# Kernel tuning notes

Measured on AMD Instinct MI355X. Metric: run time of the kernel, lower is better.

Reference implementation:

```python
import jax, jax.numpy as jnp
import numpy as np

B, T, D = 32, 1024, 512
H = 1024          # hidden_size
LV = 128          # level_hidden_size
NREP = H // LV    # n_repeat = 8
NL = 2            # num_layers


def setup_inputs() -> dict:
    key = jax.random.key(0)
    ks = jax.random.split(key, 9)
    s = 0.02
    inp = {"x": jax.random.normal(ks[0], (B, T, D), jnp.float32)}
    # layer 0: input dim D; layer 1: input dim H
    inp["W_lstm0"] = jax.random.normal(ks[1], (4 * H, D + H), jnp.float32) * s
    inp["b_lstm0"] = jnp.zeros((4 * H,), jnp.float32)
    inp["W_lvl0"] = jax.random.normal(ks[2], (2 * LV, D + H), jnp.float32) * s
    inp["b_lvl0"] = jnp.zeros((2 * LV,), jnp.float32)
    inp["W_lstm1"] = jax.random.normal(ks[3], (4 * H, H + H), jnp.float32) * s
    inp["b_lstm1"] = jnp.zeros((4 * H,), jnp.float32)
    inp["W_lvl1"] = jax.random.normal(ks[4], (2 * LV, H + H), jnp.float32) * s
    inp["b_lvl1"] = jnp.zeros((2 * LV,), jnp.float32)
    return inp


def _cell(Wl, bl, Wv, bv, h, c, x_t):
    comb = jnp.concatenate([x_t, h], axis=-1)               # [B, in+H]
    gates = comb @ Wl.T + bl                                 # [B, 4H]
    cc_i, cc_f, cc_o, cc_g = jnp.split(gates, 4, axis=-1)
    lvl = comb @ Wv.T + bv                                   # [B, 2*LV]
    cc_i_h, cc_f_h = jnp.split(lvl, 2, axis=-1)
    i = jax.nn.sigmoid(cc_i)
    f = jax.nn.sigmoid(cc_f)
    o = jax.nn.sigmoid(cc_o)
    g = jnp.tanh(cc_g)
    p_f = jax.nn.softmax(cc_f_h, axis=-1)
    p_i = jax.nn.softmax(cc_i_h[..., ::-1], axis=-1)
    i_h = jnp.cumsum(p_f, axis=-1)                           # master input gate
    f_h = jnp.cumsum(p_i, axis=-1)[..., ::-1]                # master forget gate
    i_h = jnp.repeat(i_h, NREP, axis=-1)                     # [B, H]
    f_h = jnp.repeat(f_h, NREP, axis=-1)
    w = i_h * f_h
    c_new = w * (f * c + i * g) + (f_h - w) * c + (i_h - w) * g
    h_new = o * jnp.tanh(c_new)
    return h_new, c_new


def _run_layer(Wl, bl, Wv, bv, x):
    # x: [B, T, in]
    bsz = x.shape[0]
    h0 = jnp.zeros((bsz, H), x.dtype)
    c0 = jnp.zeros((bsz, H), x.dtype)

    def step(carry, x_t):
        h, c = carry
        h, c = _cell(Wl, bl, Wv, bv, h, c, x_t)
        return (h, c), h

    (_, _), hs = jax.lax.scan(step, (h0, c0), jnp.swapaxes(x, 0, 1))
    return jnp.swapaxes(hs, 0, 1)                            # [B, T, H]


def reference(x, W_lstm0, b_lstm0, W_lvl0, b_lvl0,
              W_lstm1, b_lstm1, W_lvl1, b_lvl1):
    out0 = _run_layer(W_lstm0, b_lstm0, W_lvl0, b_lvl0, x)
    out1 = _run_layer(W_lstm1, b_lstm1, W_lvl1, b_lvl1, out0)
    return out1
```

## Files before the change

kernel.cpp:

```cpp
#include <hip/hip_runtime.h>

namespace {
constexpr int kB  = 32;
constexpr int kT  = 1024;
constexpr int kD  = 512;
constexpr int kH  = 1024;
constexpr int kLV = 128;
constexpr int kNG = 4 * kH + 2 * kLV;
constexpr int kNBLK = 256;
constexpr int kNTHR = 512;
constexpr int kOffH0 = 8192;
constexpr int kOffWF = kOffH0 + 2 * kB * kH + 2 * kB * kNG;
constexpr int kRedOff = 3 * 1536 * 2 * 16;
constexpr int kIhOff  = kRedOff + 6144;
constexpr int kFhOff  = kIhOff + 512;
constexpr int kSmxOff = kFhOff + 512;
constexpr int kLdsBytes = kSmxOff + 32;
}

typedef float vfloat4 __attribute__((ext_vector_type(4)));
typedef float floatx4 __attribute__((ext_vector_type(4)));
typedef _Float16 half8_t __attribute__((ext_vector_type(8)));
typedef unsigned short ushort_t;

static __device__ __forceinline__ unsigned ld_flag(const unsigned* p) {
  return __hip_atomic_load(p, __ATOMIC_RELAXED, __HIP_MEMORY_SCOPE_AGENT);
}
static __device__ __forceinline__ void st_flag(unsigned* p, unsigned v) {
  __hip_atomic_store(p, v, __ATOMIC_RELAXED, __HIP_MEMORY_SCOPE_AGENT);
}
static __device__ __forceinline__ float ld_coh(const float* p) {
  return __hip_atomic_load(p, __ATOMIC_RELAXED, __HIP_MEMORY_SCOPE_AGENT);
}
static __device__ __forceinline__ void st_wt(float* p, float v) {
  asm volatile("global_store_dword %0, %1, off sc0 sc1" :: "v"(p), "v"(v) : "memory");
}
static __device__ __forceinline__ void st_wtu(unsigned* p, unsigned v) {
  asm volatile("global_store_dword %0, %1, off sc0 sc1" :: "v"(p), "v"(v) : "memory");
}
static __device__ __forceinline__ void ld8h(uint4 v[8], const ushort_t* b) {
  asm volatile(
      "global_load_dwordx4 %0, %8, off sc0 sc1\n\t"
      "global_load_dwordx4 %1, %8, off offset:256 sc0 sc1\n\t"
      "global_load_dwordx4 %2, %8, off offset:512 sc0 sc1\n\t"
      "global_load_dwordx4 %3, %8, off offset:768 sc0 sc1\n\t"
      "global_load_dwordx4 %4, %8, off offset:1024 sc0 sc1\n\t"
      "global_load_dwordx4 %5, %8, off offset:1280 sc0 sc1\n\t"
      "global_load_dwordx4 %6, %8, off offset:1536 sc0 sc1\n\t"
      "global_load_dwordx4 %7, %8, off offset:1792 sc0 sc1\n\t"
      "s_waitcnt vmcnt(0)"
      : "=&v"(v[0]), "=&v"(v[1]), "=&v"(v[2]), "=&v"(v[3]),
        "=&v"(v[4]), "=&v"(v[5]), "=&v"(v[6]), "=&v"(v[7])
      : "v"(b)
      : "memory");
}
static __device__ __forceinline__ void ld8h2(uint4 v[8], uint4 w[8],
                                             const ushort_t* b0, const ushort_t* b1) {
  asm volatile(
      "global_load_dwordx4 %0,  %16, off sc0 sc1\n\t"
      "global_load_dwordx4 %1,  %16, off offset:256 sc0 sc1\n\t"
      "global_load_dwordx4 %2,  %16, off offset:512 sc0 sc1\n\t"
      "global_load_dwordx4 %3,  %16, off offset:768 sc0 sc1\n\t"
      "global_load_dwordx4 %4,  %16, off offset:1024 sc0 sc1\n\t"
      "global_load_dwordx4 %5,  %16, off offset:1280 sc0 sc1\n\t"
      "global_load_dwordx4 %6,  %16, off offset:1536 sc0 sc1\n\t"
      "global_load_dwordx4 %7,  %16, off offset:1792 sc0 sc1\n\t"
      "global_load_dwordx4 %8,  %17, off sc0 sc1\n\t"
      "global_load_dwordx4 %9,  %17, off offset:256 sc0 sc1\n\t"
      "global_load_dwordx4 %10, %17, off offset:512 sc0 sc1\n\t"
      "global_load_dwordx4 %11, %17, off offset:768 sc0 sc1\n\t"
      "global_load_dwordx4 %12, %17, off offset:1024 sc0 sc1\n\t"
      "global_load_dwordx4 %13, %17, off offset:1280 sc0 sc1\n\t"
      "global_load_dwordx4 %14, %17, off offset:1536 sc0 sc1\n\t"
      "global_load_dwordx4 %15, %17, off offset:1792 sc0 sc1\n\t"
      "s_waitcnt vmcnt(0)"
      : "=&v"(v[0]), "=&v"(v[1]), "=&v"(v[2]), "=&v"(v[3]),
        "=&v"(v[4]), "=&v"(v[5]), "=&v"(v[6]), "=&v"(v[7]),
        "=&v"(w[0]), "=&v"(w[1]), "=&v"(w[2]), "=&v"(w[3]),
        "=&v"(w[4]), "=&v"(w[5]), "=&v"(w[6]), "=&v"(w[7])
      : "v"(b0), "v"(b1)
      : "memory");
}
static __device__ __forceinline__ unsigned pkrtz(float a, float b) {
  return __builtin_bit_cast(unsigned, __builtin_amdgcn_cvt_pkrtz(a, b));
}
static __device__ __forceinline__ uint4 pack2(vfloat4 a, vfloat4 b) {
  uint4 r;
  r.x = pkrtz(a.x, a.y); r.y = pkrtz(a.z, a.w);
  r.z = pkrtz(b.x, b.y); r.w = pkrtz(b.z, b.w);
  return r;
}
static __device__ __forceinline__ floatx4 mfma16(uint4 a, uint4 b, floatx4 c) {
  return __builtin_amdgcn_mfma_f32_16x16x32_f16(
      __builtin_bit_cast(half8_t, a), __builtin_bit_cast(half8_t, b), c, 0, 0, 0);
}

__global__ __launch_bounds__(256) void cvt_fp16_kernel(
    const float* __restrict__ src, ushort_t* __restrict__ dst, int n8) {
  int i = blockIdx.x * 256 + threadIdx.x;
  if (i >= n8) return;
  const vfloat4* s4 = (const vfloat4*)src;
  vfloat4 a = s4[2 * i], b = s4[2 * i + 1];
  typedef _Float16 h8 __attribute__((ext_vector_type(8)));
  h8 o;
  o[0] = (_Float16)a.x; o[1] = (_Float16)a.y;
  o[2] = (_Float16)a.z; o[3] = (_Float16)a.w;
  o[4] = (_Float16)b.x; o[5] = (_Float16)b.y;
  o[6] = (_Float16)b.z; o[7] = (_Float16)b.w;
  ((h8*)dst)[i] = o;
}

__global__ __launch_bounds__(kNTHR, 2) void onlstm_kernel(
    const float* __restrict__ x,
    const float* __restrict__ bl0, const float* __restrict__ bv0,
    const float* __restrict__ bl1, const float* __restrict__ bv1,
    const ushort_t* __restrict__ wf0u, const ushort_t* __restrict__ wf1u,
    float* __restrict__ out, float* __restrict__ ws)
{
  const int tid = threadIdx.x;
  const int bid = blockIdx.x;

  unsigned* flags = (unsigned*)ws;
  unsigned* genp  = (unsigned*)ws + 4096;
  ushort_t* h0f = (ushort_t*)(ws + kOffH0);
  ushort_t* h1f = h0f + kB * kH;
  float* gates0 = ws + kOffH0 + kB * kH;
  float* gates1 = gates0 + kB * kNG;

  __shared__ __align__(16) char sb[kLdsBytes];
  uint4* wb4   = (uint4*)sb;
  float* redp  = (float*)(sb + kRedOff);
  float* ih_sh = (float*)(sb + kIhOff);
  float* fh_sh = (float*)(sb + kFhOff);
  float* smx   = (float*)(sb + kSmxOff);

  unsigned seq = 0;
  auto gridbar = [&]() {
    ++seq;
    asm volatile("s_waitcnt vmcnt(0)" ::: "memory");
    __syncthreads();
    if (bid == 0) {
      if (tid >= 1 && tid < kNBLK) {
        while (ld_flag(&flags[tid * 16]) != seq) __builtin_amdgcn_s_sleep(2);
      }
      __syncthreads();
      if (tid == 0) st_flag(genp, seq);
    } else {
      if (tid == 0) {
        st_flag(&flags[bid * 16], seq);
        while (ld_flag(genp) != seq) __builtin_amdgcn_s_sleep(2);
      }
      __syncthreads();
    }
    asm volatile("" ::: "memory");
  };

  int L, ntile, cb0;
  if (bid < 32)       { L = 0; ntile = 3; cb0 = bid * 48; }
  else if (bid < 120) { L = 0; ntile = 2; cb0 = 1536 + (bid - 32) * 32; }
  else                { L = 1; ntile = 2; cb0 = (bid - 120) * 32; }
  const int K   = L ? 2048 : 1536;
  const int ts4 = K * 2;
  const bool three = (ntile == 3);
  const ushort_t* wf = L ? wf1u : wf0u;
  const float* blp = L ? bl1 : bl0;
  const float* bvp = L ? bv1 : bv0;
  float* gatesL = L ? gates1 : gates0;

  const int lane = tid & 63;
  const int rt   = (tid >> 6) & 1;
  const int str  = tid >> 7;
  const int r_   = rt * 16 + (lane & 15);
  const int koct = lane >> 4;
  const int colg0 = cb0 + (lane & 15);
  const int colg1 = cb0 + 16 + (lane & 15);
  const int colg2 = cb0 + 32 + (lane & 15);

  for (int tt = 0; tt < ntile; ++tt) {
    const int colb = cb0 + tt * 16;
    for (int idx = tid; idx < ts4; idx += kNTHR) {
      int m = idx >> 6, l2 = idx & 63;
      size_t off = (size_t)(colb + (l2 & 15)) * K + m * 32 + 8 * (l2 >> 4);
      wb4[tt * ts4 + idx] = *(const uint4*)(wf + off);
    }
  }
  const float b0w = (colg0 < 4096) ? blp[colg0] : bvp[colg0 - 4096];
  const float b1w = (colg1 < 4096) ? blp[colg1] : bvp[colg1 - 4096];
  const float b2w = three ? ((colg2 < 4096) ? blp[colg2] : bvp[colg2 - 4096]) : 0.f;
  __syncthreads();

  { int idx = bid * kNTHR + tid; if (idx < kB * kH) st_wtu((unsigned*)h0f + idx, 0u); }
  float creg = 0.f;
  gridbar();

  const int pbB  = (bid & 127) >> 2;
  const int qq4B = bid & 3;
  auto cellB = [&](const float* gbase, ushort_t* hb, float& cr, float* outp, int t) {
    const float* gr = gbase + (size_t)pbB * kNG;
    const int wl = tid & 63, wv2 = tid >> 6;
    const bool sm = tid < 128;
    const bool cl = tid < 256;
    float vi = 0.f, vf = 0.f, vo = 0.f, vg = 0.f;
    int j = qq4B * 256 + tid;
    if (cl) {
      vi = ld_coh(gr + j);
      vf = ld_coh(gr + kH + j);
      vo = ld_coh(gr + 2 * kH + j);
      vg = ld_coh(gr + 3 * kH + j);
    }
    float ai = 0.f, af = 0.f;
    if (sm) { ai = ld_coh(gr + 4096 + tid); af = ld_coh(gr + 4096 + kLV + tid); }
    float mi = ai, mf = af;
    if (sm) {
#pragma unroll
      for (int d2 = 32; d2 > 0; d2 >>= 1) {
        mi = fmaxf(mi, __shfl_xor(mi, d2));
        mf = fmaxf(mf, __shfl_xor(mf, d2));
      }
      if (wl == 0) { smx[wv2] = mi; smx[2 + wv2] = mf; }
    }
    __syncthreads();
    mi = fmaxf(smx[0], smx[1]);
    mf = fmaxf(smx[2], smx[3]);
    float ei = 0.f, Pi = 0.f, Pf = 0.f;
    if (sm) {
      ei = __expf(ai - mi);
      float ef = __expf(af - mf);
      Pi = ei; Pf = ef;
#pragma unroll
      for (int d2 = 1; d2 < 64; d2 <<= 1) {
        float ni = __shfl_up(Pi, d2);
        float nf = __shfl_up(Pf, d2);
        if (wl >= d2) { Pi += ni; Pf += nf; }
      }
      if (wl == 63) { smx[4 + wv2] = Pi; smx[6 + wv2] = Pf; }
    }
    __syncthreads();
    float Si = smx[4] + smx[5], Sf = smx[6] + smx[7];
    if (sm) {
      if (wv2 == 1) { Pi += smx[4]; Pf += smx[6]; }
      ih_sh[tid] = Pf / Sf;
      fh_sh[tid] = (Si - Pi + ei) / Si;
    }
    __syncthreads();
    if (cl) {
      float i_ = 1.f / (1.f + __expf(-vi));
      float f_ = 1.f / (1.f + __expf(-vf));
      float o_ = 1.f / (1.f + __expf(-vo));
      float g_ = tanhf(vg);
      int l2 = j >> 3;
      float ih = ih_sh[l2], fh = fh_sh[l2];
      float w  = ih * fh;
      float cold = cr;
      float cn = w * (f_ * cold + i_ * g_) + (fh - w) * cold + (ih - w) * g_;
      float hn = o_ * tanhf(cn);
      cr = cn;
      float hnn = __shfl_xor(hn, 1);
      if (!(tid & 1))
        st_wtu((unsigned*)hb + ((size_t)pbB * kH + j) / 2, pkrtz(hn, hnn));
      if (outp) st_wt(outp + ((size_t)pbB * kT + t) * kH + j, hn);
    }
  };

  for (int e = 0; e <= kT; ++e) {
    const bool actA = L ? (e >= 1) : (e < kT);

    if (actA) {
      floatx4 a0 = {0.f,0.f,0.f,0.f}, a1 = a0, a2 = a0;
      if (L == 0) {
        {
          const float* bx = x + ((size_t)r_ * kT + e) * kD + str * 32 + koct * 8;
          vfloat4 vx[8];
#pragma unroll
          for (int j = 0; j < 4; ++j) {
            vx[2*j]   = *(const vfloat4*)(bx + j * 128);
            vx[2*j+1] = *(const vfloat4*)(bx + j * 128 + 4);
          }
          uint4 pa[4];
#pragma unroll
          for (int j = 0; j < 4; ++j) pa[j] = pack2(vx[2*j], vx[2*j+1]);
#pragma unroll
          for (int j = 0; j < 4; ++j) {
            const int m = str + 4 * j;
            a0 = mfma16(pa[j], wb4[m * 64 + lane], a0);
            a1 = mfma16(pa[j], wb4[ts4 + m * 64 + lane], a1);
            if (three) a2 = mfma16(pa[j], wb4[2 * ts4 + m * 64 + lane], a2);
          }
        }
        {
          uint4 pa[8];
          ld8h(pa, h0f + (size_t)r_ * kH + str * 32 + koct * 8);
#pragma unroll
          for (int j = 0; j < 8; ++j) {
            const int m = 16 + str + 4 * j;
            a0 = mfma16(pa[j], wb4[m * 64 + lane], a0);
            a1 = mfma16(pa[j], wb4[ts4 + m * 64 + lane], a1);
            if (three) a2 = mfma16(pa[j], wb4[2 * ts4 + m * 64 + lane], a2);
          }
        }
      } else {
        uint4 pa[8], pb[8];
        ld8h2(pa, pb, h0f + (size_t)r_ * kH + str * 32 + koct * 8,
                      h1f + (size_t)r_ * kH + str * 32 + koct * 8);
#pragma unroll
        for (int j = 0; j < 8; ++j) {
          const int m = str + 4 * j;
          a0 = mfma16(pa[j], wb4[m * 64 + lane], a0);
          a1 = mfma16(pa[j], wb4[ts4 + m * 64 + lane], a1);
        }
#pragma unroll
        for (int j = 0; j < 8; ++j) {
          const int m = 32 + str + 4 * j;
          a0 = mfma16(pb[j], wb4[m * 64 + lane], a0);
          a1 = mfma16(pb[j], wb4[ts4 + m * 64 + lane], a1);
        }
      }
      for (int s2 = 1; s2 < 4; ++s2) {
        if (str == s2) {
          *(floatx4*)&redp[((rt * 3 + 0) * 64 + lane) * 4] = a0;
          *(floatx4*)&redp[((rt * 3 + 1) * 64 + lane) * 4] = a1;
          if (three) *(floatx4*)&redp[((rt * 3 + 2) * 64 + lane) * 4] = a2;
        }
        __syncthreads();
        if (str == 0) {
          a0 += *(const floatx4*)&redp[((rt * 3 + 0) * 64 + lane) * 4];
          a1 += *(const floatx4*)&redp[((rt * 3 + 1) * 64 + lane) * 4];
          if (three) a2 += *(const floatx4*)&redp[((rt * 3 + 2) * 64 + lane) * 4];
        }
        __syncthreads();
      }
      if (str == 0) {
        const int rb = rt * 16 + koct * 4;
#pragma unroll
        for (int r = 0; r < 4; ++r)
          st_wt(gatesL + (size_t)(rb + r) * kNG + colg0, a0[r] + b0w);
#pragma unroll
        for (int r = 0; r < 4; ++r)
          st_wt(gatesL + (size_t)(rb + r) * kNG + colg1, a1[r] + b1w);
        if (three) {
#pragma unroll
          for (int r = 0; r < 4; ++r)
            st_wt(gatesL + (size_t)(rb + r) * kNG + colg2, a2[r] + b2w);
        }
      }
    }
    gridbar();

    if (bid < 128) {
      if (e < kT) cellB(gates0, h0f, creg, nullptr, e);
    } else {
      if (e >= 1) cellB(gates1, h1f, creg, out, e - 1);
    }
    gridbar();
  }
}

extern "C" void kernel_launch(void* const* d_in, const int* in_sizes, int n_in,
                              void* d_out, int out_size, void* d_ws, size_t ws_size,
                              hipStream_t stream) {
  const float* x   = (const float*)d_in[0];
  const float* Wl0 = (const float*)d_in[1];
  const float* bl0 = (const float*)d_in[2];
  const float* Wv0 = (const float*)d_in[3];
  const float* bv0 = (const float*)d_in[4];
  const float* Wl1 = (const float*)d_in[5];
  const float* bl1 = (const float*)d_in[6];
  const float* Wv1 = (const float*)d_in[7];
  const float* bv1 = (const float*)d_in[8];
  (void)in_sizes; (void)n_in; (void)out_size; (void)ws_size;

  float* ws = (float*)d_ws;
  ushort_t* wf0 = (ushort_t*)(ws + kOffWF);
  ushort_t* wf1 = wf0 + (size_t)4352 * 1536;

  {
    int n;
    n = 4096 * 1536 / 8;
    cvt_fp16_kernel<<<(n + 255) / 256, 256, 0, stream>>>(Wl0, wf0, n);
    n = 256 * 1536 / 8;
    cvt_fp16_kernel<<<(n + 255) / 256, 256, 0, stream>>>(
        Wv0, wf0 + (size_t)4096 * 1536, n);
    n = 4096 * 2048 / 8;
    cvt_fp16_kernel<<<(n + 255) / 256, 256, 0, stream>>>(Wl1, wf1, n);
    n = 256 * 2048 / 8;
    cvt_fp16_kernel<<<(n + 255) / 256, 256, 0, stream>>>(
        Wv1, wf1 + (size_t)4096 * 2048, n);
  }

  onlstm_kernel<<<dim3(kNBLK), dim3(kNTHR), 0, stream>>>(
      x, bl0, bv0, bl1, bv1, wf0, wf1, (float*)d_out, ws);
}
```

Baseline: 11.12 ms.

## Replace centralized grid barrier with per-block flag waits on dependent subsets

The single master-block grid barrier is replaced with per-block signal flags. Each block now polls only the flags of the blocks whose outputs it depends on: layer-0 GEMM blocks wait on the layer-0 cell blocks, and layer-1 blocks wait on all blocks or on layer-1 gate producers. This removes the two-hop gather-then-broadcast latency and some unnecessary waits each timestep. Separately, the cross-wave partial-sum reduction now uses multiple LDS slots so three waves write at once instead of serializing across three barrier rounds, at the cost of a doubled reduction buffer. Correctness relies on the dependency subsets and monotonic flag values being exactly right.

```diff
diff --git a/kernel.cpp b/kernel.cpp
--- a/kernel.cpp
+++ b/kernel.cpp
@@ -12,7 +12,7 @@
 constexpr int kOffH0 = 8192;
 constexpr int kOffWF = kOffH0 + 2 * kB * kH + 2 * kB * kNG;
 constexpr int kRedOff = 3 * 1536 * 2 * 16;
-constexpr int kIhOff  = kRedOff + 6144;
+constexpr int kIhOff  = kRedOff + 12288;
 constexpr int kFhOff  = kIhOff + 512;
 constexpr int kSmxOff = kFhOff + 512;
 constexpr int kLdsBytes = kSmxOff + 32;
@@ -120,8 +120,8 @@
   const int tid = threadIdx.x;
   const int bid = blockIdx.x;
 
-  unsigned* flags = (unsigned*)ws;
-  unsigned* genp  = (unsigned*)ws + 4096;
+  unsigned* flagA = (unsigned*)ws;
+  unsigned* flagB = (unsigned*)ws + 4096;
   ushort_t* h0f = (ushort_t*)(ws + kOffH0);
   ushort_t* h1f = h0f + kB * kH;
   float* gates0 = ws + kOffH0 + kB * kH;
@@ -134,24 +134,17 @@
   float* fh_sh = (float*)(sb + kFhOff);
   float* smx   = (float*)(sb + kSmxOff);
 
-  unsigned seq = 0;
-  auto gridbar = [&]() {
-    ++seq;
+  auto signal = [&](unsigned* arr, unsigned v) {
     asm volatile("s_waitcnt vmcnt(0)" ::: "memory");
     __syncthreads();
-    if (bid == 0) {
-      if (tid >= 1 && tid < kNBLK) {
-        while (ld_flag(&flags[tid * 16]) != seq) __builtin_amdgcn_s_sleep(2);
-      }
-      __syncthreads();
-      if (tid == 0) st_flag(genp, seq);
-    } else {
-      if (tid == 0) {
-        st_flag(&flags[bid * 16], seq);
-        while (ld_flag(genp) != seq) __builtin_amdgcn_s_sleep(2);
-      }
-      __syncthreads();
-    }
+    if (tid == 0) st_flag(&arr[bid * 16], v);
+  };
+  auto wait_set = [&](unsigned* arr, int lo, int n, unsigned target) {
+    if (tid < n) {
+      while (ld_flag(&arr[(lo + tid) * 16]) != target)
+        __builtin_amdgcn_s_sleep(2);
+    }
+    __syncthreads();
     asm volatile("" ::: "memory");
   };
 
@@ -162,6 +155,7 @@
   const int K   = L ? 2048 : 1536;
   const int ts4 = K * 2;
   const bool three = (ntile == 3);
+  const int rstride = three ? 3 : 2;
   const ushort_t* wf = L ? wf1u : wf0u;
   const float* blp = L ? bl1 : bl0;
   const float* bvp = L ? bv1 : bv0;
@@ -176,6 +170,10 @@
   const int colg1 = cb0 + 16 + (lane & 15);
   const int colg2 = cb0 + 32 + (lane & 15);
 
+  auto redsl = [&](int slot, int accIdx) -> float* {
+    return &redp[(((slot * 2 + rt) * rstride) + accIdx) * 256 + lane * 4];
+  };
+
   for (int tt = 0; tt < ntile; ++tt) {
     const int colb = cb0 + tt * 16;
     for (int idx = tid; idx < ts4; idx += kNTHR) {
@@ -191,7 +189,9 @@
 
   { int idx = bid * kNTHR + tid; if (idx < kB * kH) st_wtu((unsigned*)h0f + idx, 0u); }
   float creg = 0.f;
-  gridbar();
+  signal(flagB, 1u);
+  if (bid < 120) wait_set(flagB, 0, 128, 1u);
+  else           wait_set(flagB, 0, 256, 1u);
 
   const int pbB  = (bid & 127) >> 2;
   const int qq4B = bid & 3;
@@ -315,19 +315,46 @@
           a1 = mfma16(pb[j], wb4[ts4 + m * 64 + lane], a1);
         }
       }
-      for (int s2 = 1; s2 < 4; ++s2) {
-        if (str == s2) {
-          *(floatx4*)&redp[((rt * 3 + 0) * 64 + lane) * 4] = a0;
-          *(floatx4*)&redp[((rt * 3 + 1) * 64 + lane) * 4] = a1;
-          if (three) *(floatx4*)&redp[((rt * 3 + 2) * 64 + lane) * 4] = a2;
+      if (!three) {
+        if (str != 0) {
+          *(floatx4*)redsl(str - 1, 0) = a0;
+          *(floatx4*)redsl(str - 1, 1) = a1;
         }
         __syncthreads();
         if (str == 0) {
-          a0 += *(const floatx4*)&redp[((rt * 3 + 0) * 64 + lane) * 4];
-          a1 += *(const floatx4*)&redp[((rt * 3 + 1) * 64 + lane) * 4];
-          if (three) a2 += *(const floatx4*)&redp[((rt * 3 + 2) * 64 + lane) * 4];
+#pragma unroll
+          for (int s2 = 0; s2 < 3; ++s2) {
+            a0 += *(const floatx4*)redsl(s2, 0);
+            a1 += *(const floatx4*)redsl(s2, 1);
+          }
+        }
+      } else {
+        if (str == 1 || str == 2) {
+          *(floatx4*)redsl(str - 1, 0) = a0;
+          *(floatx4*)redsl(str - 1, 1) = a1;
+          *(floatx4*)redsl(str - 1, 2) = a2;
         }
         __syncthreads();
+        if (str == 0) {
+#pragma unroll
+          for (int s2 = 0; s2 < 2; ++s2) {
+            a0 += *(const floatx4*)redsl(s2, 0);
+            a1 += *(const floatx4*)redsl(s2, 1);
+            a2 += *(const floatx4*)redsl(s2, 2);
+          }
+        }
+        __syncthreads();
+        if (str == 3) {
+          *(floatx4*)redsl(0, 0) = a0;
+          *(floatx4*)redsl(0, 1) = a1;
+          *(floatx4*)redsl(0, 2) = a2;
+        }
+        __syncthreads();
+        if (str == 0) {
+          a0 += *(const floatx4*)redsl(0, 0);
+          a1 += *(const floatx4*)redsl(0, 1);
+          a2 += *(const floatx4*)redsl(0, 2);
+        }
       }
       if (str == 0) {
         const int rb = rt * 16 + koct * 4;
@@ -344,14 +371,20 @@
         }
       }
     }
-    gridbar();
+    signal(flagA, (unsigned)(e + 1));
+    if (bid < 128) wait_set(flagA, 0, 256, (unsigned)(e + 1));
+    else           wait_set(flagA, 120, 136, (unsigned)(e + 1));
 
     if (bid < 128) {
       if (e < kT) cellB(gates0, h0f, creg, nullptr, e);
     } else {
       if (e >= 1) cellB(gates1, h1f, creg, out, e - 1);
     }
-    gridbar();
+    signal(flagB, (unsigned)(e + 2));
+    if (e < kT) {
+      if (bid < 120) wait_set(flagB, 0, 128, (unsigned)(e + 2));
+      else           wait_set(flagB, 0, 256, (unsigned)(e + 2));
+    }
   }
 }
 
```

After: 10.88 ms. -2.2%, faster.
